# Performance work log

Hardware: AMD Instinct MI355X
Metric: run time of the kernel (lower is better)

Reference implementation:

```python
import jax, jax.numpy as jnp
import numpy as np

RATIO = 1.0   # dense_feature_matching is called with ratio_th=1 in match()
EPS = 1e-8


def setup_inputs() -> dict:
    key = jax.random.key(0)
    kA, kB = jax.random.split(key)
    D, N1, N2 = 704, 8192, 8192
    map_A = jax.random.normal(kA, (D, N1), dtype=jnp.float32)
    map_B = jax.random.normal(kB, (D, N2), dtype=jnp.float32)
    return {"map_A": map_A, "map_B": map_B}


def _mnn_ratio_match(d1, d2, ratio, bidirectional=True):
    # d1: [N1, D] L2-normalized, d2: [N2, D] L2-normalized
    sim = d1 @ d2.T                                   # [N1, N2]
    # forward direction: top-2 over columns
    s12, i12 = jax.lax.top_k(sim, 2)                   # [N1, 2]
    dist12 = 2.0 - 2.0 * s12
    ratios12 = dist12[:, 0] / (dist12[:, 1] + EPS)
    nn12 = i12[:, 0]
    match_sim = s12[:, 0]
    # backward direction: top-2 over rows (of sim) == columns of sim.T
    s21, i21 = jax.lax.top_k(sim.T, 2)                 # [N2, 2]
    dist21 = 2.0 - 2.0 * s21
    ratios21 = dist21[:, 0] / (dist21[:, 1] + EPS)
    if not bidirectional:
        ratios21 = ratios21 * 0.0
    nn21 = i21[:, 0]
    ids1 = jnp.arange(sim.shape[0])
    mask = (ids1 == nn21[nn12]) & (ratios12 <= ratio) & (ratios21[nn12] <= ratio)
    # fixed-shape (jit-safe) encoding of the variable-length match list:
    # unmatched rows get index -1 and similarity 0.
    matches = jnp.stack([ids1, nn12], axis=-1)          # [N1, 2]
    matches = jnp.where(mask[:, None], matches, -1)
    match_sim = jnp.where(mask, match_sim, 0.0)
    return matches, match_sim, mask


def reference(map_A, map_B):
    # dense_feature_matching: transpose to [N, D] and L2-normalize rows
    d1 = map_A.T
    d1 = d1 / jnp.sqrt(jnp.sum(jnp.square(d1), axis=1, keepdims=True))
    d2 = map_B.T
    d2 = d2 / jnp.sqrt(jnp.sum(jnp.square(d2), axis=1, keepdims=True))
    matches, match_sim, mask = _mnn_ratio_match(d1, d2, RATIO, bidirectional=True)
    return matches, match_sim, mask
```

## Files before the change

kernel.cpp:

```cpp
#include <hip/hip_runtime.h>
#include <stdint.h>
#include <math.h>

typedef _Float16 f16;
typedef _Float16 f16x8 __attribute__((ext_vector_type(8)));
typedef float f32x4 __attribute__((ext_vector_type(4)));

#define KD 704
#define NPTS 8192

typedef const unsigned __attribute__((address_space(1)))* gas_ptr;
typedef unsigned __attribute__((address_space(3)))* las_ptr;

__device__ inline void gld16(const void* g, void* l) {
  __builtin_amdgcn_global_load_lds((gas_ptr)g, (las_ptr)l, 16, 0, 0);
}

__device__ inline unsigned long long packkey(float v, int idx) {
  unsigned b = __float_as_uint(v);
  b ^= ((unsigned)((int)b >> 31)) | 0x80000000u;
  return ((unsigned long long)b << 32) | (unsigned)(~idx);
}

__global__ void k_norm_init(const float* __restrict__ A, const float* __restrict__ B,
                            float* __restrict__ invA, float* __restrict__ invB,
                            unsigned long long* rowbest, unsigned long long* colbest) {
  int g = blockIdx.x * 256 + threadIdx.x;
  const float* M = (g < NPTS) ? A : B;
  int c = g & (NPTS - 1);
  float ss = 0.f;
  for (int d = 0; d < KD; ++d) {
    float x = M[(size_t)d * NPTS + c];
    ss = fmaf(x, x, ss);
  }
  float inv = 256.0f / sqrtf(ss);
  if (g < NPTS) { invA[c] = inv; rowbest[c] = 0ull; }
  else          { invB[c] = inv; colbest[c] = 0ull; }
}

__global__ void k_split(const float* __restrict__ A, const float* __restrict__ B,
                        const float* __restrict__ invA, const float* __restrict__ invB,
                        f16* __restrict__ Ahi, f16* __restrict__ Alo,
                        f16* __restrict__ Bhi, f16* __restrict__ Blo) {
  __shared__ float t[32][33];
  int z = blockIdx.z;
  const float* M   = z ? B    : A;
  const float* inv = z ? invB : invA;
  f16* Hi = z ? Bhi : Ahi;
  f16* Lo = z ? Blo : Alo;
  int c0 = blockIdx.x * 32, d0 = blockIdx.y * 32;
  int tx = threadIdx.x & 31, ty = threadIdx.x >> 5;
  #pragma unroll
  for (int s = 0; s < 4; ++s)
    t[ty + s * 8][tx] = M[(size_t)(d0 + ty + s * 8) * NPTS + (c0 + tx)];
  __syncthreads();
  #pragma unroll
  for (int s = 0; s < 4; ++s) {
    int i = c0 + ty + s * 8;
    float v = t[tx][ty + s * 8] * inv[i];
    f16 hi = (f16)v;
    f16 lo = (f16)(v - (float)hi);
    size_t o = (size_t)i * KD + (d0 + tx);
    Hi[o] = hi;
    Lo[o] = lo;
  }
}

__global__ __launch_bounds__(256, 2)
void k_gemm_top1(const f16* __restrict__ Ahi, const f16* __restrict__ Alo,
                 const f16* __restrict__ Bhi, const f16* __restrict__ Blo,
                 unsigned long long* rowbest, unsigned long long* colbest) {
  __shared__ f16 sAh[128 * 64];
  __shared__ f16 sAl[128 * 64];
  __shared__ f16 sBh[128 * 64];
  __shared__ f16 sBl[128 * 64];

  const int tid = threadIdx.x, lane = tid & 63, wave = tid >> 6;
  const int bj = blockIdx.x & 63, bi = blockIdx.x >> 6;
  const int wr = wave >> 1, wc = wave & 1;

  f32x4 acc[4][4] = {};

  const int srow = wave * 32 + (lane >> 3);
  const int cs   = ((lane & 7) ^ (srow & 7)) * 16;
  const size_t rowbytes = (size_t)KD * 2;
  const char* pAh = (const char*)Ahi + (size_t)(bi * 128 + srow) * rowbytes + cs;
  const char* pAl = (const char*)Alo + (size_t)(bi * 128 + srow) * rowbytes + cs;
  const char* pBh = (const char*)Bhi + (size_t)(bj * 128 + srow) * rowbytes + cs;
  const char* pBl = (const char*)Blo + (size_t)(bj * 128 + srow) * rowbytes + cs;
  const unsigned lbase = wave * 4096;

  for (int ks = 0; ks < 11; ++ks) {
    const size_t kb = (size_t)ks * 128;
    #pragma unroll
    for (int q = 0; q < 4; ++q) {
      size_t go = kb + (size_t)q * 8 * rowbytes;
      unsigned lo_ = lbase + q * 1024;
      gld16(pAh + go, (char*)sAh + lo_);
      gld16(pAl + go, (char*)sAl + lo_);
      gld16(pBh + go, (char*)sBh + lo_);
      gld16(pBl + go, (char*)sBl + lo_);
    }
    __syncthreads();

    #pragma unroll
    for (int kk = 0; kk < 2; ++kk) {
      f16x8 ah[4], al[4], bh[4], bl[4];
      const int sa = ((kk * 4 + (lane >> 4)) ^ (lane & 7)) * 16;
      #pragma unroll
      for (int a = 0; a < 4; ++a) {
        int row = wr * 64 + a * 16 + (lane & 15);
        ah[a] = *(const f16x8*)((const char*)sAh + row * 128 + sa);
        al[a] = *(const f16x8*)((const char*)sAl + row * 128 + sa);
      }
      #pragma unroll
      for (int b = 0; b < 4; ++b) {
        int row = wc * 64 + b * 16 + (lane & 15);
        bh[b] = *(const f16x8*)((const char*)sBh + row * 128 + sa);
        bl[b] = *(const f16x8*)((const char*)sBl + row * 128 + sa);
      }
      #pragma unroll
      for (int a = 0; a < 4; ++a)
        #pragma unroll
        for (int b = 0; b < 4; ++b) {
          acc[a][b] = __builtin_amdgcn_mfma_f32_16x16x32_f16(ah[a], bh[b], acc[a][b], 0, 0, 0);
          acc[a][b] = __builtin_amdgcn_mfma_f32_16x16x32_f16(ah[a], bl[b], acc[a][b], 0, 0, 0);
          acc[a][b] = __builtin_amdgcn_mfma_f32_16x16x32_f16(al[a], bh[b], acc[a][b], 0, 0, 0);
        }
    }
    __syncthreads();
  }

  const float scale = 1.0f / 65536.0f;
  const int R0 = bi * 128 + wr * 64;
  const int C0 = bj * 128 + wc * 64;

  #pragma unroll
  for (int a = 0; a < 4; ++a) {
    #pragma unroll
    for (int r = 0; r < 4; ++r) {
      float bv = acc[a][0][r];
      int bjx = C0 + (lane & 15);
      #pragma unroll
      for (int b = 1; b < 4; ++b) {
        float v = acc[a][b][r];
        if (v > bv) { bv = v; bjx = C0 + b * 16 + (lane & 15); }
      }
      unsigned long long key = packkey(bv * scale, bjx);
      #pragma unroll
      for (int off = 1; off < 16; off <<= 1) {
        unsigned long long o = __shfl_xor(key, off);
        if (o > key) key = o;
      }
      if ((lane & 15) == 0) {
        int row = R0 + a * 16 + (lane >> 4) * 4 + r;
        atomicMax(&rowbest[row], key);
      }
    }
  }
  #pragma unroll
  for (int b = 0; b < 4; ++b) {
    unsigned long long key = 0ull;
    #pragma unroll
    for (int a = 0; a < 4; ++a)
      #pragma unroll
      for (int r = 0; r < 4; ++r) {
        int i = R0 + a * 16 + (lane >> 4) * 4 + r;
        unsigned long long k2 = packkey(acc[a][b][r] * scale, i);
        if (k2 > key) key = k2;
      }
    unsigned long long o = __shfl_xor(key, 16); if (o > key) key = o;
    o = __shfl_xor(key, 32); if (o > key) key = o;
    if (lane < 16) atomicMax(&colbest[C0 + b * 16 + lane], key);
  }
}

__global__ void k_epilogue(const unsigned long long* __restrict__ rowbest,
                           const unsigned long long* __restrict__ colbest,
                           float* __restrict__ out) {
  int i = blockIdx.x * 256 + threadIdx.x;
  unsigned long long rk = rowbest[i];
  int j = (int)(~(unsigned)rk);
  unsigned hb = (unsigned)(rk >> 32);
  hb ^= (hb >> 31) ? 0x80000000u : 0xFFFFFFFFu;
  float sim = __uint_as_float(hb);
  unsigned long long ck = colbest[j];
  int nn21 = (int)(~(unsigned)ck);
  bool m = (nn21 == i);
  out[2 * i]     = m ? (float)i : -1.0f;
  out[2 * i + 1] = m ? (float)j : -1.0f;
  out[2 * NPTS + i] = m ? sim : 0.0f;
  out[3 * NPTS + i] = m ? 1.0f : 0.0f;
}

extern "C" void kernel_launch(void* const* d_in, const int* in_sizes, int n_in,
                              void* d_out, int out_size, void* d_ws, size_t ws_size,
                              hipStream_t stream) {
  const float* A = (const float*)d_in[0];
  const float* B = (const float*)d_in[1];
  char* ws = (char*)d_ws;

  const size_t SPLIT = (size_t)NPTS * KD * 2;
  unsigned long long* rowbest = (unsigned long long*)(ws);
  unsigned long long* colbest = (unsigned long long*)(ws + 65536);
  float* invA = (float*)(ws + 131072);
  float* invB = (float*)(ws + 163840);
  f16* Ahi = (f16*)(ws + 196608);
  f16* Alo = (f16*)(ws + 196608 + SPLIT);
  f16* Bhi = (f16*)(ws + 196608 + 2 * SPLIT);
  f16* Blo = (f16*)(ws + 196608 + 3 * SPLIT);

  k_norm_init<<<64, 256, 0, stream>>>(A, B, invA, invB, rowbest, colbest);
  dim3 g2(NPTS / 32, KD / 32, 2);
  k_split<<<g2, 256, 0, stream>>>(A, B, invA, invB, Ahi, Alo, Bhi, Blo);
  k_gemm_top1<<<4096, 256, 0, stream>>>(Ahi, Alo, Bhi, Blo, rowbest, colbest);
  k_epilogue<<<NPTS / 256, 256, 0, stream>>>(rowbest, colbest, (float*)d_out);
}
```

Measured before the change: 436.0 us.

## Restructure split-fp16 GEMM into 256x256 double-buffered pipelined tiles with swizzled grid

The GEMM kernel becomes 512-thread blocks on 256x256 output tiles. The three hi/lo product terms are treated as 33 sequential K-stages over a double-buffered LDS, with async global-to-LDS loads interleaved with MFMA phases and setprio hints. Block order is swizzled for L2 reuse. The norm kernel now splits the reduction over 8 thread groups and zeroes rowbest/colbest through one contiguous slot array, and the split kernel writes two elements per thread. The aims are to hide load latency and raise the compute-to-load ratio, at the cost of more register pressure and a fragile hand-written waitcnt schedule.

After: 475.9 us. 1.09x slower.

```diff
diff --git a/kernel.cpp b/kernel.cpp
--- a/kernel.cpp
+++ b/kernel.cpp
@@ -8,34 +8,46 @@
 
 #define KD 704
 #define NPTS 8192
+#define ROWB 1408
 
 typedef const unsigned __attribute__((address_space(1)))* gas_ptr;
 typedef unsigned __attribute__((address_space(3)))* las_ptr;
 
-__device__ inline void gld16(const void* g, void* l) {
+__device__ __forceinline__ void gld16(const void* g, void* l) {
   __builtin_amdgcn_global_load_lds((gas_ptr)g, (las_ptr)l, 16, 0, 0);
 }
 
-__device__ inline unsigned long long packkey(float v, int idx) {
+__device__ __forceinline__ unsigned long long packkey(float v, int idx) {
   unsigned b = __float_as_uint(v);
   b ^= ((unsigned)((int)b >> 31)) | 0x80000000u;
   return ((unsigned long long)b << 32) | (unsigned)(~idx);
 }
 
-__global__ void k_norm_init(const float* __restrict__ A, const float* __restrict__ B,
-                            float* __restrict__ invA, float* __restrict__ invB,
-                            unsigned long long* rowbest, unsigned long long* colbest) {
-  int g = blockIdx.x * 256 + threadIdx.x;
-  const float* M = (g < NPTS) ? A : B;
-  int c = g & (NPTS - 1);
+__global__ void k_norm(const float* __restrict__ A, const float* __restrict__ B,
+                       float* __restrict__ invA, float* __restrict__ invB,
+                       unsigned long long* __restrict__ slots) {
+  __shared__ float p[256];
+  const int blk = blockIdx.x;
+  const int mat = blk >> 8;
+  const float* M = mat ? B : A;
+  float* inv = mat ? invB : invA;
+  const int cbase = (blk & 255) << 5;
+  const int c = cbase + (threadIdx.x & 31);
+  const int s = threadIdx.x >> 5;
   float ss = 0.f;
-  for (int d = 0; d < KD; ++d) {
+  for (int d = s; d < KD; d += 8) {
     float x = M[(size_t)d * NPTS + c];
     ss = fmaf(x, x, ss);
   }
-  float inv = 256.0f / sqrtf(ss);
-  if (g < NPTS) { invA[c] = inv; rowbest[c] = 0ull; }
-  else          { invB[c] = inv; colbest[c] = 0ull; }
+  p[threadIdx.x] = ss;
+  if (blk < 64) slots[blk * 256 + threadIdx.x] = 0ull;
+  __syncthreads();
+  if (threadIdx.x < 32) {
+    float t = 0.f;
+    #pragma unroll
+    for (int k = 0; k < 8; ++k) t += p[k * 32 + threadIdx.x];
+    inv[cbase + threadIdx.x] = 256.0f / sqrtf(t);
+  }
 }
 
 __global__ void k_split(const float* __restrict__ A, const float* __restrict__ B,
@@ -43,127 +55,222 @@
                         f16* __restrict__ Ahi, f16* __restrict__ Alo,
                         f16* __restrict__ Bhi, f16* __restrict__ Blo) {
   __shared__ float t[32][33];
-  int z = blockIdx.z;
+  const int z = blockIdx.z;
   const float* M   = z ? B    : A;
   const float* inv = z ? invB : invA;
   f16* Hi = z ? Bhi : Ahi;
   f16* Lo = z ? Blo : Alo;
-  int c0 = blockIdx.x * 32, d0 = blockIdx.y * 32;
-  int tx = threadIdx.x & 31, ty = threadIdx.x >> 5;
+  const int c0 = blockIdx.x * 32, d0 = blockIdx.y * 32;
+  const int tx = threadIdx.x & 31, ty = threadIdx.x >> 5;
   #pragma unroll
   for (int s = 0; s < 4; ++s)
     t[ty + s * 8][tx] = M[(size_t)(d0 + ty + s * 8) * NPTS + (c0 + tx)];
   __syncthreads();
+  const int tx16 = threadIdx.x & 15, ty16 = threadIdx.x >> 4;
   #pragma unroll
-  for (int s = 0; s < 4; ++s) {
-    int i = c0 + ty + s * 8;
-    float v = t[tx][ty + s * 8] * inv[i];
-    f16 hi = (f16)v;
-    f16 lo = (f16)(v - (float)hi);
-    size_t o = (size_t)i * KD + (d0 + tx);
-    Hi[o] = hi;
-    Lo[o] = lo;
-  }
-}
-
-__global__ __launch_bounds__(256, 2)
-void k_gemm_top1(const f16* __restrict__ Ahi, const f16* __restrict__ Alo,
-                 const f16* __restrict__ Bhi, const f16* __restrict__ Blo,
-                 unsigned long long* rowbest, unsigned long long* colbest) {
-  __shared__ f16 sAh[128 * 64];
-  __shared__ f16 sAl[128 * 64];
-  __shared__ f16 sBh[128 * 64];
-  __shared__ f16 sBl[128 * 64];
-
-  const int tid = threadIdx.x, lane = tid & 63, wave = tid >> 6;
-  const int bj = blockIdx.x & 63, bi = blockIdx.x >> 6;
-  const int wr = wave >> 1, wc = wave & 1;
-
-  f32x4 acc[4][4] = {};
-
-  const int srow = wave * 32 + (lane >> 3);
-  const int cs   = ((lane & 7) ^ (srow & 7)) * 16;
-  const size_t rowbytes = (size_t)KD * 2;
-  const char* pAh = (const char*)Ahi + (size_t)(bi * 128 + srow) * rowbytes + cs;
-  const char* pAl = (const char*)Alo + (size_t)(bi * 128 + srow) * rowbytes + cs;
-  const char* pBh = (const char*)Bhi + (size_t)(bj * 128 + srow) * rowbytes + cs;
-  const char* pBl = (const char*)Blo + (size_t)(bj * 128 + srow) * rowbytes + cs;
-  const unsigned lbase = wave * 4096;
-
-  for (int ks = 0; ks < 11; ++ks) {
-    const size_t kb = (size_t)ks * 128;
-    #pragma unroll
-    for (int q = 0; q < 4; ++q) {
-      size_t go = kb + (size_t)q * 8 * rowbytes;
-      unsigned lo_ = lbase + q * 1024;
-      gld16(pAh + go, (char*)sAh + lo_);
-      gld16(pAl + go, (char*)sAl + lo_);
-      gld16(pBh + go, (char*)sBh + lo_);
-      gld16(pBl + go, (char*)sBl + lo_);
-    }
-    __syncthreads();
-
-    #pragma unroll
-    for (int kk = 0; kk < 2; ++kk) {
-      f16x8 ah[4], al[4], bh[4], bl[4];
-      const int sa = ((kk * 4 + (lane >> 4)) ^ (lane & 7)) * 16;
-      #pragma unroll
-      for (int a = 0; a < 4; ++a) {
-        int row = wr * 64 + a * 16 + (lane & 15);
-        ah[a] = *(const f16x8*)((const char*)sAh + row * 128 + sa);
-        al[a] = *(const f16x8*)((const char*)sAl + row * 128 + sa);
-      }
-      #pragma unroll
-      for (int b = 0; b < 4; ++b) {
-        int row = wc * 64 + b * 16 + (lane & 15);
-        bh[b] = *(const f16x8*)((const char*)sBh + row * 128 + sa);
-        bl[b] = *(const f16x8*)((const char*)sBl + row * 128 + sa);
-      }
-      #pragma unroll
-      for (int a = 0; a < 4; ++a)
-        #pragma unroll
-        for (int b = 0; b < 4; ++b) {
-          acc[a][b] = __builtin_amdgcn_mfma_f32_16x16x32_f16(ah[a], bh[b], acc[a][b], 0, 0, 0);
-          acc[a][b] = __builtin_amdgcn_mfma_f32_16x16x32_f16(ah[a], bl[b], acc[a][b], 0, 0, 0);
-          acc[a][b] = __builtin_amdgcn_mfma_f32_16x16x32_f16(al[a], bh[b], acc[a][b], 0, 0, 0);
-        }
-    }
-    __syncthreads();
+  for (int s2 = 0; s2 < 2; ++s2) {
+    const int i = c0 + ty16 + s2 * 16;
+    const float iv = inv[i];
+    const float v0 = t[tx16 * 2][ty16 + s2 * 16] * iv;
+    const float v1 = t[tx16 * 2 + 1][ty16 + s2 * 16] * iv;
+    const f16 h0 = (f16)v0, h1 = (f16)v1;
+    const f16 l0 = (f16)(v0 - (float)h0), l1 = (f16)(v1 - (float)h1);
+    const size_t o = (size_t)i * KD + d0 + tx16 * 2;
+    Hi[o] = h0; Hi[o + 1] = h1;
+    Lo[o] = l0; Lo[o + 1] = l1;
+  }
+}
+
+__global__ __launch_bounds__(512, 2)
+void k_gemm_top1(const f16* __restrict__ Ah_, const f16* __restrict__ Al_,
+                 const f16* __restrict__ Bh_, const f16* __restrict__ Bl_,
+                 unsigned long long* __restrict__ rowbest,
+                 unsigned long long* __restrict__ colbest) {
+  __shared__ f16 sA[2][256][64];
+  __shared__ f16 sB[2][256][64];
+
+  const int tid = threadIdx.x;
+  const int lane = tid & 63, w = tid >> 6;
+  const int wr = w >> 2, wc = w & 3;
+
+  const int lin = blockIdx.x;
+  const int swz = (lin & 7) * 128 + (lin >> 3);
+  const int bi = swz >> 5, bj = swz & 31;
+
+  const char* Ah = (const char*)Ah_;
+  const char* Al = (const char*)Al_;
+  const char* Bh = (const char*)Bh_;
+  const char* Bl = (const char*)Bl_;
+  const size_t arow = (size_t)(bi * 256) * ROWB;
+  const size_t brow = (size_t)(bj * 256) * ROWB;
+
+  const int inv_g = (w * 8 + (lane >> 3)) * ROWB + ((((lane & 7) ^ ((lane >> 3) & 7))) << 4);
+  char* const lA = (char*)&sA[0][0][0] + w * 1024;
+  char* const lB = (char*)&sB[0][0][0] + w * 1024;
+
+#define STAGEH(srcbase, tilerow, ko, ldsroot, buf, h)                                  \
+  do {                                                                                 \
+    const char* g0_ = (srcbase) + (tilerow) + (size_t)(h) * (128 * (size_t)ROWB) +     \
+                      (size_t)(ko) + inv_g;                                            \
+    char* l0_ = (ldsroot) + (buf) * 32768 + (h) * 16384;                               \
+    gld16(g0_, l0_);                                                                   \
+    gld16(g0_ + (size_t)64 * ROWB, l0_ + 8192);                                        \
+  } while (0)
+
+#define TSEL(X, sa_, sb_, ko_)                                                         \
+  do {                                                                                 \
+    int rg_ = ((X) >= 22) ? 2 : (((X) >= 11) ? 1 : 0);                                 \
+    sa_ = (rg_ == 2) ? Al : Ah;                                                        \
+    sb_ = (rg_ == 1) ? Bl : Bh;                                                        \
+    ko_ = ((X) - rg_ * 11) * 128;                                                      \
+  } while (0)
+
+  const int rA0 = (wr * 128 + (lane & 15)) * 128;
+  const int rB0 = (wc * 64 + (lane & 15)) * 128;
+  const int x0 = (((lane >> 4)) ^ (lane & 7)) << 4;
+  const int x1 = ((4 + (lane >> 4)) ^ (lane & 7)) << 4;
+
+  f32x4 acc[8][4] = {};
+  f16x8 ar[4][2], br[4][2];
+
+  {
+    const char *sa, *sb; int ko;
+    TSEL(0, sa, sb, ko);
+    STAGEH(sa, arow, ko, lA, 0, 0);
+    STAGEH(sa, arow, ko, lA, 0, 1);
+    STAGEH(sb, brow, ko, lB, 0, 0);
+    STAGEH(sb, brow, ko, lB, 0, 1);
+    TSEL(1, sa, sb, ko);
+    STAGEH(sa, arow, ko, lA, 1, 0);
+    STAGEH(sa, arow, ko, lA, 1, 1);
+    STAGEH(sb, brow, ko, lB, 1, 0);
+  }
+  asm volatile("s_waitcnt vmcnt(6)" ::: "memory");
+  __builtin_amdgcn_sched_barrier(0);
+  __builtin_amdgcn_s_barrier();
+
+#pragma unroll 1
+  for (int T = 0; T < 33; ++T) {
+    const int cur = T & 1;
+    const char* sAc = (const char*)&sA[0][0][0] + cur * 32768;
+    const char* sBc = (const char*)&sB[0][0][0] + cur * 32768;
+
+#pragma unroll
+    for (int a = 0; a < 4; ++a) {
+      ar[a][0] = *(const f16x8*)(sAc + rA0 + a * 2048 + x0);
+      ar[a][1] = *(const f16x8*)(sAc + rA0 + a * 2048 + x1);
+    }
+#pragma unroll
+    for (int b = 0; b < 2; ++b) {
+      br[b][0] = *(const f16x8*)(sBc + rB0 + b * 2048 + x0);
+      br[b][1] = *(const f16x8*)(sBc + rB0 + b * 2048 + x1);
+    }
+    if (T + 1 <= 32) {
+      const char *sa, *sb; int ko;
+      TSEL(T + 1, sa, sb, ko);
+      STAGEH(sb, brow, ko, lB, cur ^ 1, 1);
+    }
+    __builtin_amdgcn_s_barrier();
+    __builtin_amdgcn_s_setprio(1);
+#pragma unroll
+    for (int a = 0; a < 4; ++a)
+#pragma unroll
+      for (int b = 0; b < 2; ++b) {
+        acc[a][b] = __builtin_amdgcn_mfma_f32_16x16x32_f16(ar[a][0], br[b][0], acc[a][b], 0, 0, 0);
+        acc[a][b] = __builtin_amdgcn_mfma_f32_16x16x32_f16(ar[a][1], br[b][1], acc[a][b], 0, 0, 0);
+      }
+    __builtin_amdgcn_s_setprio(0);
+    __builtin_amdgcn_s_barrier();
+
+#pragma unroll
+    for (int b = 2; b < 4; ++b) {
+      br[b][0] = *(const f16x8*)(sBc + rB0 + b * 2048 + x0);
+      br[b][1] = *(const f16x8*)(sBc + rB0 + b * 2048 + x1);
+    }
+    __builtin_amdgcn_s_setprio(1);
+#pragma unroll
+    for (int a = 0; a < 4; ++a)
+#pragma unroll
+      for (int b = 2; b < 4; ++b) {
+        acc[a][b] = __builtin_amdgcn_mfma_f32_16x16x32_f16(ar[a][0], br[b][0], acc[a][b], 0, 0, 0);
+        acc[a][b] = __builtin_amdgcn_mfma_f32_16x16x32_f16(ar[a][1], br[b][1], acc[a][b], 0, 0, 0);
+      }
+    __builtin_amdgcn_s_setprio(0);
+    __builtin_amdgcn_s_barrier();
+
+#pragma unroll
+    for (int a = 0; a < 4; ++a) {
+      ar[a][0] = *(const f16x8*)(sAc + rA0 + (a + 4) * 2048 + x0);
+      ar[a][1] = *(const f16x8*)(sAc + rA0 + (a + 4) * 2048 + x1);
+    }
+    __builtin_amdgcn_s_setprio(1);
+#pragma unroll
+    for (int a = 0; a < 4; ++a)
+#pragma unroll
+      for (int b = 0; b < 2; ++b) {
+        acc[a + 4][b] = __builtin_amdgcn_mfma_f32_16x16x32_f16(ar[a][0], br[b][0], acc[a + 4][b], 0, 0, 0);
+        acc[a + 4][b] = __builtin_amdgcn_mfma_f32_16x16x32_f16(ar[a][1], br[b][1], acc[a + 4][b], 0, 0, 0);
+      }
+    __builtin_amdgcn_s_setprio(0);
+    __builtin_amdgcn_s_barrier();
+
+    if (T + 2 <= 32) {
+      const char *sa, *sb; int ko;
+      TSEL(T + 2, sa, sb, ko);
+      STAGEH(sa, arow, ko, lA, cur, 0);
+      STAGEH(sa, arow, ko, lA, cur, 1);
+      STAGEH(sb, brow, ko, lB, cur, 0);
+    }
+    __builtin_amdgcn_s_setprio(1);
+#pragma unroll
+    for (int a = 0; a < 4; ++a)
+#pragma unroll
+      for (int b = 2; b < 4; ++b) {
+        acc[a + 4][b] = __builtin_amdgcn_mfma_f32_16x16x32_f16(ar[a][0], br[b][0], acc[a + 4][b], 0, 0, 0);
+        acc[a + 4][b] = __builtin_amdgcn_mfma_f32_16x16x32_f16(ar[a][1], br[b][1], acc[a + 4][b], 0, 0, 0);
+      }
+    __builtin_amdgcn_s_setprio(0);
+    if (T < 31) {
+      asm volatile("s_waitcnt vmcnt(6)" ::: "memory");
+    } else {
+      asm volatile("s_waitcnt vmcnt(0)" ::: "memory");
+    }
+    __builtin_amdgcn_sched_barrier(0);
+    __builtin_amdgcn_s_barrier();
   }
 
   const float scale = 1.0f / 65536.0f;
-  const int R0 = bi * 128 + wr * 64;
-  const int C0 = bj * 128 + wc * 64;
-
-  #pragma unroll
-  for (int a = 0; a < 4; ++a) {
-    #pragma unroll
+  const int R0 = bi * 256 + wr * 128;
+  const int C0 = bj * 256 + wc * 64;
+
+#pragma unroll
+  for (int a = 0; a < 8; ++a) {
+#pragma unroll
     for (int r = 0; r < 4; ++r) {
       float bv = acc[a][0][r];
       int bjx = C0 + (lane & 15);
-      #pragma unroll
+#pragma unroll
       for (int b = 1; b < 4; ++b) {
         float v = acc[a][b][r];
         if (v > bv) { bv = v; bjx = C0 + b * 16 + (lane & 15); }
       }
       unsigned long long key = packkey(bv * scale, bjx);
-      #pragma unroll
+#pragma unroll
       for (int off = 1; off < 16; off <<= 1) {
         unsigned long long o = __shfl_xor(key, off);
         if (o > key) key = o;
       }
       if ((lane & 15) == 0) {
-        int row = R0 + a * 16 + (lane >> 4) * 4 + r;
-        atomicMax(&rowbest[row], key);
-      }
-    }
-  }
-  #pragma unroll
+        atomicMax(&rowbest[R0 + a * 16 + (lane >> 4) * 4 + r], key);
+      }
+    }
+  }
+#pragma unroll
   for (int b = 0; b < 4; ++b) {
     unsigned long long key = 0ull;
-    #pragma unroll
-    for (int a = 0; a < 4; ++a)
-      #pragma unroll
+#pragma unroll
+    for (int a = 0; a < 8; ++a)
+#pragma unroll
       for (int r = 0; r < 4; ++r) {
         int i = R0 + a * 16 + (lane >> 4) * 4 + r;
         unsigned long long k2 = packkey(acc[a][b][r] * scale, i);
@@ -173,6 +280,8 @@
     o = __shfl_xor(key, 32); if (o > key) key = o;
     if (lane < 16) atomicMax(&colbest[C0 + b * 16 + lane], key);
   }
+#undef STAGEH
+#undef TSEL
 }
 
 __global__ void k_epilogue(const unsigned long long* __restrict__ rowbest,
@@ -210,9 +319,9 @@
   f16* Bhi = (f16*)(ws + 196608 + 2 * SPLIT);
   f16* Blo = (f16*)(ws + 196608 + 3 * SPLIT);
 
-  k_norm_init<<<64, 256, 0, stream>>>(A, B, invA, invB, rowbest, colbest);
+  k_norm<<<512, 256, 0, stream>>>(A, B, invA, invB, rowbest );
   dim3 g2(NPTS / 32, KD / 32, 2);
   k_split<<<g2, 256, 0, stream>>>(A, B, invA, invB, Ahi, Alo, Bhi, Blo);
-  k_gemm_top1<<<4096, 256, 0, stream>>>(Ahi, Alo, Bhi, Blo, rowbest, colbest);
+  k_gemm_top1<<<1024, 512, 0, stream>>>(Ahi, Alo, Bhi, Blo, rowbest, colbest);
   k_epilogue<<<NPTS / 256, 256, 0, stream>>>(rowbest, colbest, (float*)d_out);
 }
```
